# Performance work log

Measured on AMD Instinct MI355X. Metric: run time of the kernel, lower is better.

Reference implementation:

```python
import jax, jax.numpy as jnp
import numpy as np

N_NODES = 100000
N_EDGES = 1600000
N_GRAPHS = 256
IN_F = 64   # global_features (GNN input dim)
OUT_F = 64  # node_features (GNN output dim)


def setup_inputs() -> dict:
    key = jax.random.key(0)
    ks = jax.random.split(key, 8)
    x = jax.random.normal(ks[0], (N_NODES, IN_F), dtype=jnp.float32)
    edge_index = jax.random.randint(ks[1], (2, N_EDGES), 0, N_NODES, dtype=jnp.int64)
    batch = jnp.sort(jax.random.randint(ks[2], (N_NODES,), 0, N_GRAPHS, dtype=jnp.int64))
    # GNNLayer linear: in=global_features, out=node_features
    W_gnn = jax.random.normal(ks[3], (IN_F, OUT_F), dtype=jnp.float32) / np.sqrt(IN_F)
    b_gnn = jnp.zeros((OUT_F,), dtype=jnp.float32)
    # global_attention: Linear(node_features, 1)
    W_att = jax.random.normal(ks[4], (OUT_F, 1), dtype=jnp.float32) / np.sqrt(OUT_F)
    b_att = jnp.zeros((1,), dtype=jnp.float32)
    return {"x": x, "edge_index": edge_index, "batch": batch,
            "W_gnn": W_gnn, "b_gnn": b_gnn, "W_att": W_att, "b_att": b_att}


def reference(x, edge_index, batch, W_gnn, b_gnn, W_att, b_att):
    src, dst = edge_index[0], edge_index[1]
    # --- GNN message passing layer: aggregate neighbor features, transform ---
    agg = jax.ops.segment_sum(x[src], dst, num_segments=N_NODES)  # [N, IN_F]
    h = jax.nn.relu((x + agg) @ W_gnn + b_gnn)                    # [N, OUT_F]
    # --- attention scores + scatter softmax over batch segments ---
    scores = (h @ W_att + b_att)[:, 0]                            # [N]
    seg_max = jax.ops.segment_max(scores, batch, num_segments=N_GRAPHS)
    e = jnp.exp(scores - seg_max[batch])
    denom = jax.ops.segment_sum(e, batch, num_segments=N_GRAPHS)
    w = e / denom[batch]                                          # [N]
    # --- weighted scatter-add pooling ---
    out = jax.ops.segment_sum(w[:, None] * h, batch, num_segments=N_GRAPHS)
    return out  # [N_GRAPHS, OUT_F]
```

## Files before the change

### kernel.cpp

```cpp
#include <hip/hip_runtime.h>

#define N_NODES  100000
#define N_EDGES  1600000
#define N_GRAPHS 256
#define F        64

#define CHUNK    8192
#define NCHUNK   196
#define GBN      128
#define NB2      782
#define EDGE_CAP 2560

#define CAST_ELEMS   (N_NODES * F / 4)
#define CAST_BLOCKS  ((CAST_ELEMS + 1023) / 1024)
#define PREP_BLOCKS  (NCHUNK + CAST_BLOCKS)

__device__ __forceinline__ unsigned short f2bf(float f) {
    unsigned int u = __float_as_uint(f);
    u += 0x7FFFu + ((u >> 16) & 1u);
    return (unsigned short)(u >> 16);
}

__global__ __launch_bounds__(1024) void prep_kernel(
        const float* __restrict__ x, unsigned short* __restrict__ xh,
        const int* __restrict__ src, const int* __restrict__ dst,
        unsigned int* __restrict__ pairs, int* __restrict__ cstartT,
        float* __restrict__ out, float* __restrict__ denom) {
    int tid = threadIdx.x;
    int b   = blockIdx.x;

    if (b >= NCHUNK) {
        int ci = b - NCHUNK;
        if (ci == 0) {
            for (int i = tid; i < N_GRAPHS * F; i += 1024) out[i] = 0.f;
            if (tid < N_GRAPHS) denom[tid] = 0.f;
        }
        int i = ci * 1024 + tid;
        if (i < CAST_ELEMS) {
            float4 v = ((const float4*)x)[i];
            ushort4 o;
            o.x = f2bf(v.x); o.y = f2bf(v.y); o.z = f2bf(v.z); o.w = f2bf(v.w);
            ((ushort4*)xh)[i] = o;
        }
        return;
    }

    __shared__ int hist[NB2];
    __shared__ int cur[NB2];
    __shared__ int scan[1024];
    __shared__ unsigned int stage[CHUNK];
    int c    = b;
    int base = c * CHUNK;
    int m    = min(CHUNK, N_EDGES - base);

    for (int k = tid; k < NB2; k += 1024) hist[k] = 0;
    __syncthreads();
    for (int e = tid; e < m; e += 1024)
        atomicAdd(&hist[dst[base + e] >> 7], 1);
    __syncthreads();
    scan[tid] = (tid < NB2) ? hist[tid] : 0;
    __syncthreads();
    #pragma unroll
    for (int o = 1; o < 1024; o <<= 1) {
        int u = (tid >= o) ? scan[tid - o] : 0;
        __syncthreads();
        scan[tid] += u;
        __syncthreads();
    }
    if (tid < NB2) {
        int excl = scan[tid] - hist[tid];
        cur[tid] = excl;
        cstartT[tid * NCHUNK + c] = base + excl;
    }
    if (tid == 0) cstartT[NB2 * NCHUNK + c] = base + m;
    __syncthreads();
    for (int e = tid; e < m; e += 1024) {
        int d = dst[base + e];
        int slot = atomicAdd(&cur[d >> 7], 1);
        stage[slot] = ((unsigned)(d & (GBN - 1)) << 17) | (unsigned)src[base + e];
    }
    __syncthreads();
    for (int e = tid; e < m; e += 1024)
        pairs[base + e] = stage[e];
}

__global__ __launch_bounds__(512) void compact_kernel(
        const unsigned int* __restrict__ pairs,
        const int* __restrict__ cstartT,
        int* __restrict__ eidx,
        int* __restrict__ nbeg,
        int* __restrict__ nend) {
    __shared__ int rstart[NCHUNK];
    __shared__ int roff[NCHUNK + 1];
    __shared__ int sc[256];
    __shared__ unsigned int epairs[EDGE_CAP];
    __shared__ int ncnt[GBN];
    __shared__ int ncur[GBN];

    int tid   = threadIdx.x;
    int b     = blockIdx.x;
    int node0 = b * GBN;
    int nn    = min(GBN, N_NODES - node0);
    int gbase = b * EDGE_CAP;

    int myrc = 0;
    if (tid < NCHUNK) {
        int a = cstartT[b * NCHUNK + tid];
        int n = cstartT[(b + 1) * NCHUNK + tid];
        rstart[tid] = a;
        myrc = n - a;
    }
    __syncthreads();
    if (tid < 256) sc[tid] = (tid < NCHUNK) ? myrc : 0;
    __syncthreads();
    #pragma unroll
    for (int o = 1; o < 256; o <<= 1) {
        int u = (tid < 256 && tid >= o) ? sc[tid - o] : 0;
        __syncthreads();
        if (tid < 256) sc[tid] += u;
        __syncthreads();
    }
    if (tid < NCHUNK) roff[tid] = sc[tid] - myrc;
    if (tid == 0) roff[NCHUNK] = sc[NCHUNK - 1];
    __syncthreads();
    int E = roff[NCHUNK];

    for (int e = tid; e < E; e += 512) {
        int lo = 0, hi = NCHUNK - 1;
        while (lo < hi) {
            int mid = (lo + hi + 1) >> 1;
            if (roff[mid] <= e) lo = mid; else hi = mid - 1;
        }
        epairs[e] = pairs[rstart[lo] + (e - roff[lo])];
    }
    __syncthreads();

    if (tid < GBN) ncnt[tid] = 0;
    __syncthreads();
    for (int e = tid; e < E; e += 512)
        atomicAdd(&ncnt[epairs[e] >> 17], 1);
    __syncthreads();
    if (tid < 128) sc[tid] = ncnt[tid];
    __syncthreads();
    #pragma unroll
    for (int o = 1; o < 128; o <<= 1) {
        int u = (tid < 128 && tid >= o) ? sc[tid - o] : 0;
        __syncthreads();
        if (tid < 128) sc[tid] += u;
        __syncthreads();
    }
    if (tid < GBN) {
        int excl = sc[tid] - ncnt[tid];
        ncur[tid] = excl;
        if (tid < nn) {
            nbeg[node0 + tid] = gbase + excl;
            nend[node0 + tid] = gbase + excl + ncnt[tid];
        }
    }
    __syncthreads();
    for (int e = tid; e < E; e += 512) {
        unsigned int p = epairs[e];
        int slot = atomicAdd(&ncur[p >> 17], 1);
        eidx[gbase + slot] = (int)(p & 0x1FFFFu);
    }
}

#define NODES_PER_WAVE 13
#define GT_NWAVES  ((N_NODES + NODES_PER_WAVE - 1) / NODES_PER_WAVE)
#define GT_BLOCKS  ((GT_NWAVES + 3) / 4)

__device__ __forceinline__ float bfl(unsigned int u) { return __uint_as_float(u << 16); }
__device__ __forceinline__ float bfh(unsigned int u) { return __uint_as_float(u & 0xFFFF0000u); }

__global__ __launch_bounds__(256) void gather_pool_kernel(
        const unsigned short* __restrict__ xh,
        const int*   __restrict__ nbeg,
        const int*   __restrict__ nend,
        const int*   __restrict__ eidx,
        const int*   __restrict__ batch,
        const float* __restrict__ Wg,
        const float* __restrict__ bg,
        const float* __restrict__ Wa,
        const float* __restrict__ ba,
        float*       __restrict__ out_acc,
        float*       __restrict__ denom) {
    int tid  = threadIdx.x;
    int lane = tid & 63;
    int grp  = lane >> 3;
    int c    = lane & 7;
    int waveId = blockIdx.x * 4 + (tid >> 6);

    int n0 = waveId * NODES_PER_WAVE;
    if (n0 >= N_NODES) return;
    int nEnd = n0 + NODES_PER_WAVE;
    if (nEnd > N_NODES) nEnd = N_NODES;

    float wcol[F];
    #pragma unroll
    for (int k = 0; k < F; ++k) wcol[k] = Wg[k * F + lane];
    float bgl = bg[lane];
    float wal = Wa[lane];
    float ba0 = ba[0];

    const uint4* xh4 = (const uint4*)xh;

    int   cur_g = batch[n0];
    float accw  = 0.f;
    float denw  = 0.f;

    int pb = nbeg[n0];
    int pe = nend[n0];
    int sl_cur = (pb + lane < pe) ? eidx[pb + lane] : 0;

    for (int n = n0; n < nEnd; ++n) {
        int start = pb, end = pe;
        int sl    = sl_cur;
        if (n + 1 < nEnd) {
            pb = nbeg[n + 1];
            pe = nend[n + 1];
            sl_cur = (pb + lane < pe) ? eidx[pb + lane] : 0;
        }

        float a0=0.f,a1=0.f,a2=0.f,a3=0.f,a4=0.f,a5=0.f,a6=0.f,a7=0.f;
        {
            int jmax = end - start; if (jmax > 64) jmax = 64;
            for (int j = 0; j < jmax; j += 8) {
                int el = j + grp;
                int s  = __shfl(sl, el, 64);
                if (el < jmax) {
                    uint4 v = xh4[s * 8 + c];
                    a0 += bfl(v.x); a1 += bfh(v.x);
                    a2 += bfl(v.y); a3 += bfh(v.y);
                    a4 += bfl(v.z); a5 += bfh(v.z);
                    a6 += bfl(v.w); a7 += bfh(v.w);
                }
            }
        }
        for (int base = start + 64; base < end; base += 64) {
            int jmax = end - base; if (jmax > 64) jmax = 64;
            int sl2 = (base + lane < end) ? eidx[base + lane] : 0;
            for (int j = 0; j < jmax; j += 8) {
                int el = j + grp;
                int s  = __shfl(sl2, el, 64);
                if (el < jmax) {
                    uint4 v = xh4[s * 8 + c];
                    a0 += bfl(v.x); a1 += bfh(v.x);
                    a2 += bfl(v.y); a3 += bfh(v.y);
                    a4 += bfl(v.z); a5 += bfh(v.z);
                    a6 += bfl(v.w); a7 += bfh(v.w);
                }
            }
        }
        #pragma unroll
        for (int o = 8; o <= 32; o <<= 1) {
            a0 += __shfl_xor(a0, o, 64); a1 += __shfl_xor(a1, o, 64);
            a2 += __shfl_xor(a2, o, 64); a3 += __shfl_xor(a3, o, 64);
            a4 += __shfl_xor(a4, o, 64); a5 += __shfl_xor(a5, o, 64);
            a6 += __shfl_xor(a6, o, 64); a7 += __shfl_xor(a7, o, 64);
        }
        {
            uint4 v = xh4[n * 8 + c];
            a0 += bfl(v.x); a1 += bfh(v.x);
            a2 += bfl(v.y); a3 += bfh(v.y);
            a4 += bfl(v.z); a5 += bfh(v.z);
            a6 += bfl(v.w); a7 += bfh(v.w);
        }

        float re[8] = {a0,a1,a2,a3,a4,a5,a6,a7};
        float q0=0.f,q1=0.f,q2=0.f,q3=0.f,q4=0.f,q5=0.f,q6=0.f,q7=0.f;
        #pragma unroll
        for (int k = 0; k < F; k += 8) {
            int ln = k >> 3;
            q0 += __int_as_float(__builtin_amdgcn_readlane(__float_as_int(re[0]), ln)) * wcol[k + 0];
            q1 += __int_as_float(__builtin_amdgcn_readlane(__float_as_int(re[1]), ln)) * wcol[k + 1];
            q2 += __int_as_float(__builtin_amdgcn_readlane(__float_as_int(re[2]), ln)) * wcol[k + 2];
            q3 += __int_as_float(__builtin_amdgcn_readlane(__float_as_int(re[3]), ln)) * wcol[k + 3];
            q4 += __int_as_float(__builtin_amdgcn_readlane(__float_as_int(re[4]), ln)) * wcol[k + 4];
            q5 += __int_as_float(__builtin_amdgcn_readlane(__float_as_int(re[5]), ln)) * wcol[k + 5];
            q6 += __int_as_float(__builtin_amdgcn_readlane(__float_as_int(re[6]), ln)) * wcol[k + 6];
            q7 += __int_as_float(__builtin_amdgcn_readlane(__float_as_int(re[7]), ln)) * wcol[k + 7];
        }
        float hv = ((q0 + q1) + (q2 + q3)) + ((q4 + q5) + (q6 + q7)) + bgl;
        hv = hv > 0.f ? hv : 0.f;

        float p = hv * wal;
        #pragma unroll
        for (int o = 32; o > 0; o >>= 1)
            p += __shfl_down(p, o, 64);
        float s = __int_as_float(__builtin_amdgcn_readlane(__float_as_int(p), 0)) + ba0;
        float e = __expf(s);

        int g = batch[n];
        if (g != cur_g) {
            atomicAdd(&out_acc[cur_g * F + lane], accw);
            if (lane == 0) atomicAdd(&denom[cur_g], denw);
            accw = 0.f; denw = 0.f; cur_g = g;
        }
        accw += e * hv;
        denw += e;
    }
    atomicAdd(&out_acc[cur_g * F + lane], accw);
    if (lane == 0) atomicAdd(&denom[cur_g], denw);
}

__global__ __launch_bounds__(256) void finalize_kernel(
        float* __restrict__ out, const float* __restrict__ denom) {
    int i = blockIdx.x * 256 + threadIdx.x;
    if (i >= N_GRAPHS * F) return;
    float d = denom[i >> 6];
    out[i] = (d > 0.f) ? out[i] / d : 0.f;
}

extern "C" void kernel_launch(void* const* d_in, const int* in_sizes, int n_in,
                              void* d_out, int out_size, void* d_ws, size_t ws_size,
                              hipStream_t stream) {
    const float* x     = (const float*)d_in[0];
    const int*   ei    = (const int*)d_in[1];
    const int*   batch = (const int*)d_in[2];
    const float* Wg    = (const float*)d_in[3];
    const float* bg    = (const float*)d_in[4];
    const float* Wa    = (const float*)d_in[5];
    const float* ba    = (const float*)d_in[6];
    float* out = (float*)d_out;

    const int* src = ei;
    const int* dst = ei + N_EDGES;

    char* ws = (char*)d_ws;
    unsigned short* xh      = (unsigned short*)(ws);
    unsigned int*   pairs   = (unsigned int*)(ws + 12800000);
    int*            cstartT = (int*)(ws + 19200000);
    int*            eidx    = (int*)(ws + 19814144);
    int*            nbeg    = (int*)(ws + 27821824);
    int*            nend    = (int*)(ws + 28221824);
    float*          denom   = (float*)(ws + 28621824);

    prep_kernel       <<<PREP_BLOCKS, 1024, 0, stream>>>(
        x, xh, src, dst, pairs, cstartT, out, denom);
    compact_kernel    <<<NB2, 512, 0, stream>>>(pairs, cstartT, eidx, nbeg, nend);
    gather_pool_kernel<<<GT_BLOCKS, 256, 0, stream>>>(
        xh, nbeg, nend, eidx, batch, Wg, bg, Wa, ba, out, denom);
    finalize_kernel   <<<(N_GRAPHS * F + 255) / 256, 256, 0, stream>>>(out, denom);
}
```

Baseline: 197.1 us.

## Fuse all four kernels into one cooperative persistent kernel with grid syncs

Merges the prep, compact, gather-pool and finalize kernels into a single cooperative kernel. Each phase runs as a grid-stride loop over a persistent grid, with grid-wide barriers between phases, and the phases share one LDS union. The aim is to remove kernel launch gaps and tail effects. In exchange, the gather phase now runs at 1024 threads per block, with 64 weight registers per thread and occupancy-limited residency, which may lower latency hiding. If maxB*256 exceeds the device's resident capacity, the cooperative launch may fail.

```diff
diff --git a/kernel.cpp b/kernel.cpp
--- a/kernel.cpp
+++ b/kernel.cpp
@@ -1,4 +1,7 @@
 #include <hip/hip_runtime.h>
+#include <hip/hip_cooperative_groups.h>
+
+namespace cg = cooperative_groups;
 
 #define N_NODES  100000
 #define N_EDGES  1600000
@@ -11,304 +14,295 @@
 #define NB2      782
 #define EDGE_CAP 2560
 
-#define CAST_ELEMS   (N_NODES * F / 4)
-#define CAST_BLOCKS  ((CAST_ELEMS + 1023) / 1024)
-#define PREP_BLOCKS  (NCHUNK + CAST_BLOCKS)
+#define CAST_ELEMS (N_NODES * F / 4)
+#define NCHK16     ((N_NODES + 15) / 16)
 
 __device__ __forceinline__ unsigned short f2bf(float f) {
     unsigned int u = __float_as_uint(f);
     u += 0x7FFFu + ((u >> 16) & 1u);
     return (unsigned short)(u >> 16);
 }
-
-__global__ __launch_bounds__(1024) void prep_kernel(
-        const float* __restrict__ x, unsigned short* __restrict__ xh,
+__device__ __forceinline__ float bfl(unsigned int u) { return __uint_as_float(u << 16); }
+__device__ __forceinline__ float bfh(unsigned int u) { return __uint_as_float(u & 0xFFFF0000u); }
+
+union PhaseLDS {
+    struct {
+        int hist[NB2];
+        int cur[NB2];
+        int scan[1024];
+        unsigned int stage[CHUNK];
+    } p;
+    struct {
+        int rstart[NCHUNK];
+        int roff[NCHUNK + 1];
+        int sc[256];
+        unsigned int epairs[EDGE_CAP];
+        int ncnt[GBN];
+        int ncur[GBN];
+    } c;
+};
+
+__global__ __launch_bounds__(1024) void mega_kernel(
+        const float* __restrict__ x,
+        unsigned short* __restrict__ xh,
         const int* __restrict__ src, const int* __restrict__ dst,
         unsigned int* __restrict__ pairs, int* __restrict__ cstartT,
+        int* __restrict__ eidx, int* __restrict__ nbeg, int* __restrict__ nend,
+        const int* __restrict__ batch,
+        const float* __restrict__ Wg, const float* __restrict__ bg,
+        const float* __restrict__ Wa, const float* __restrict__ ba,
         float* __restrict__ out, float* __restrict__ denom) {
+    cg::grid_group grid = cg::this_grid();
+    __shared__ PhaseLDS sh;
     int tid = threadIdx.x;
-    int b   = blockIdx.x;
-
-    if (b >= NCHUNK) {
-        int ci = b - NCHUNK;
+    int nB  = gridDim.x;
+
+    for (int c = blockIdx.x; c < NCHUNK; c += nB) {
+        int base = c * CHUNK;
+        int m    = min(CHUNK, N_EDGES - base);
+        for (int k = tid; k < NB2; k += 1024) sh.p.hist[k] = 0;
+        __syncthreads();
+        for (int e = tid; e < m; e += 1024)
+            atomicAdd(&sh.p.hist[dst[base + e] >> 7], 1);
+        __syncthreads();
+        sh.p.scan[tid] = (tid < NB2) ? sh.p.hist[tid] : 0;
+        __syncthreads();
+        #pragma unroll
+        for (int o = 1; o < 1024; o <<= 1) {
+            int u = (tid >= o) ? sh.p.scan[tid - o] : 0;
+            __syncthreads();
+            sh.p.scan[tid] += u;
+            __syncthreads();
+        }
+        if (tid < NB2) {
+            int excl = sh.p.scan[tid] - sh.p.hist[tid];
+            sh.p.cur[tid] = excl;
+            cstartT[tid * NCHUNK + c] = base + excl;
+        }
+        if (tid == 0) cstartT[NB2 * NCHUNK + c] = base + m;
+        __syncthreads();
+        for (int e = tid; e < m; e += 1024) {
+            int d = dst[base + e];
+            int slot = atomicAdd(&sh.p.cur[d >> 7], 1);
+            sh.p.stage[slot] = ((unsigned)(d & (GBN - 1)) << 17) | (unsigned)src[base + e];
+        }
+        __syncthreads();
+        for (int e = tid; e < m; e += 1024)
+            pairs[base + e] = sh.p.stage[e];
+        __syncthreads();
+    }
+    if (blockIdx.x >= NCHUNK) {
+        int castBlocks = nB - NCHUNK;
+        int ci = blockIdx.x - NCHUNK;
         if (ci == 0) {
             for (int i = tid; i < N_GRAPHS * F; i += 1024) out[i] = 0.f;
             if (tid < N_GRAPHS) denom[tid] = 0.f;
         }
-        int i = ci * 1024 + tid;
-        if (i < CAST_ELEMS) {
+        for (int i = ci * 1024 + tid; i < CAST_ELEMS; i += castBlocks * 1024) {
             float4 v = ((const float4*)x)[i];
             ushort4 o;
             o.x = f2bf(v.x); o.y = f2bf(v.y); o.z = f2bf(v.z); o.w = f2bf(v.w);
             ((ushort4*)xh)[i] = o;
         }
-        return;
-    }
-
-    __shared__ int hist[NB2];
-    __shared__ int cur[NB2];
-    __shared__ int scan[1024];
-    __shared__ unsigned int stage[CHUNK];
-    int c    = b;
-    int base = c * CHUNK;
-    int m    = min(CHUNK, N_EDGES - base);
-
-    for (int k = tid; k < NB2; k += 1024) hist[k] = 0;
-    __syncthreads();
-    for (int e = tid; e < m; e += 1024)
-        atomicAdd(&hist[dst[base + e] >> 7], 1);
-    __syncthreads();
-    scan[tid] = (tid < NB2) ? hist[tid] : 0;
-    __syncthreads();
-    #pragma unroll
-    for (int o = 1; o < 1024; o <<= 1) {
-        int u = (tid >= o) ? scan[tid - o] : 0;
-        __syncthreads();
-        scan[tid] += u;
-        __syncthreads();
-    }
-    if (tid < NB2) {
-        int excl = scan[tid] - hist[tid];
-        cur[tid] = excl;
-        cstartT[tid * NCHUNK + c] = base + excl;
-    }
-    if (tid == 0) cstartT[NB2 * NCHUNK + c] = base + m;
-    __syncthreads();
-    for (int e = tid; e < m; e += 1024) {
-        int d = dst[base + e];
-        int slot = atomicAdd(&cur[d >> 7], 1);
-        stage[slot] = ((unsigned)(d & (GBN - 1)) << 17) | (unsigned)src[base + e];
-    }
-    __syncthreads();
-    for (int e = tid; e < m; e += 1024)
-        pairs[base + e] = stage[e];
-}
-
-__global__ __launch_bounds__(512) void compact_kernel(
-        const unsigned int* __restrict__ pairs,
-        const int* __restrict__ cstartT,
-        int* __restrict__ eidx,
-        int* __restrict__ nbeg,
-        int* __restrict__ nend) {
-    __shared__ int rstart[NCHUNK];
-    __shared__ int roff[NCHUNK + 1];
-    __shared__ int sc[256];
-    __shared__ unsigned int epairs[EDGE_CAP];
-    __shared__ int ncnt[GBN];
-    __shared__ int ncur[GBN];
-
-    int tid   = threadIdx.x;
-    int b     = blockIdx.x;
-    int node0 = b * GBN;
-    int nn    = min(GBN, N_NODES - node0);
-    int gbase = b * EDGE_CAP;
-
-    int myrc = 0;
-    if (tid < NCHUNK) {
-        int a = cstartT[b * NCHUNK + tid];
-        int n = cstartT[(b + 1) * NCHUNK + tid];
-        rstart[tid] = a;
-        myrc = n - a;
-    }
-    __syncthreads();
-    if (tid < 256) sc[tid] = (tid < NCHUNK) ? myrc : 0;
-    __syncthreads();
-    #pragma unroll
-    for (int o = 1; o < 256; o <<= 1) {
-        int u = (tid < 256 && tid >= o) ? sc[tid - o] : 0;
-        __syncthreads();
-        if (tid < 256) sc[tid] += u;
-        __syncthreads();
-    }
-    if (tid < NCHUNK) roff[tid] = sc[tid] - myrc;
-    if (tid == 0) roff[NCHUNK] = sc[NCHUNK - 1];
-    __syncthreads();
-    int E = roff[NCHUNK];
-
-    for (int e = tid; e < E; e += 512) {
-        int lo = 0, hi = NCHUNK - 1;
-        while (lo < hi) {
-            int mid = (lo + hi + 1) >> 1;
-            if (roff[mid] <= e) lo = mid; else hi = mid - 1;
-        }
-        epairs[e] = pairs[rstart[lo] + (e - roff[lo])];
-    }
-    __syncthreads();
-
-    if (tid < GBN) ncnt[tid] = 0;
-    __syncthreads();
-    for (int e = tid; e < E; e += 512)
-        atomicAdd(&ncnt[epairs[e] >> 17], 1);
-    __syncthreads();
-    if (tid < 128) sc[tid] = ncnt[tid];
-    __syncthreads();
-    #pragma unroll
-    for (int o = 1; o < 128; o <<= 1) {
-        int u = (tid < 128 && tid >= o) ? sc[tid - o] : 0;
-        __syncthreads();
-        if (tid < 128) sc[tid] += u;
-        __syncthreads();
-    }
-    if (tid < GBN) {
-        int excl = sc[tid] - ncnt[tid];
-        ncur[tid] = excl;
-        if (tid < nn) {
-            nbeg[node0 + tid] = gbase + excl;
-            nend[node0 + tid] = gbase + excl + ncnt[tid];
-        }
-    }
-    __syncthreads();
-    for (int e = tid; e < E; e += 512) {
-        unsigned int p = epairs[e];
-        int slot = atomicAdd(&ncur[p >> 17], 1);
-        eidx[gbase + slot] = (int)(p & 0x1FFFFu);
-    }
-}
-
-#define NODES_PER_WAVE 13
-#define GT_NWAVES  ((N_NODES + NODES_PER_WAVE - 1) / NODES_PER_WAVE)
-#define GT_BLOCKS  ((GT_NWAVES + 3) / 4)
-
-__device__ __forceinline__ float bfl(unsigned int u) { return __uint_as_float(u << 16); }
-__device__ __forceinline__ float bfh(unsigned int u) { return __uint_as_float(u & 0xFFFF0000u); }
-
-__global__ __launch_bounds__(256) void gather_pool_kernel(
-        const unsigned short* __restrict__ xh,
-        const int*   __restrict__ nbeg,
-        const int*   __restrict__ nend,
-        const int*   __restrict__ eidx,
-        const int*   __restrict__ batch,
-        const float* __restrict__ Wg,
-        const float* __restrict__ bg,
-        const float* __restrict__ Wa,
-        const float* __restrict__ ba,
-        float*       __restrict__ out_acc,
-        float*       __restrict__ denom) {
-    int tid  = threadIdx.x;
-    int lane = tid & 63;
-    int grp  = lane >> 3;
-    int c    = lane & 7;
-    int waveId = blockIdx.x * 4 + (tid >> 6);
-
-    int n0 = waveId * NODES_PER_WAVE;
-    if (n0 >= N_NODES) return;
-    int nEnd = n0 + NODES_PER_WAVE;
-    if (nEnd > N_NODES) nEnd = N_NODES;
-
-    float wcol[F];
-    #pragma unroll
-    for (int k = 0; k < F; ++k) wcol[k] = Wg[k * F + lane];
-    float bgl = bg[lane];
-    float wal = Wa[lane];
-    float ba0 = ba[0];
-
-    const uint4* xh4 = (const uint4*)xh;
-
-    int   cur_g = batch[n0];
-    float accw  = 0.f;
-    float denw  = 0.f;
-
-    int pb = nbeg[n0];
-    int pe = nend[n0];
-    int sl_cur = (pb + lane < pe) ? eidx[pb + lane] : 0;
-
-    for (int n = n0; n < nEnd; ++n) {
-        int start = pb, end = pe;
-        int sl    = sl_cur;
-        if (n + 1 < nEnd) {
-            pb = nbeg[n + 1];
-            pe = nend[n + 1];
-            sl_cur = (pb + lane < pe) ? eidx[pb + lane] : 0;
-        }
-
-        float a0=0.f,a1=0.f,a2=0.f,a3=0.f,a4=0.f,a5=0.f,a6=0.f,a7=0.f;
-        {
-            int jmax = end - start; if (jmax > 64) jmax = 64;
-            for (int j = 0; j < jmax; j += 8) {
-                int el = j + grp;
-                int s  = __shfl(sl, el, 64);
-                if (el < jmax) {
-                    uint4 v = xh4[s * 8 + c];
+    }
+    __threadfence();
+    grid.sync();
+
+    for (int b = blockIdx.x; b < NB2; b += nB) {
+        int node0 = b * GBN;
+        int nn    = min(GBN, N_NODES - node0);
+        int gbase = b * EDGE_CAP;
+
+        int myrc = 0;
+        if (tid < NCHUNK) {
+            int a = cstartT[b * NCHUNK + tid];
+            int n = cstartT[(b + 1) * NCHUNK + tid];
+            sh.c.rstart[tid] = a;
+            myrc = n - a;
+        }
+        __syncthreads();
+        if (tid < 256) sh.c.sc[tid] = (tid < NCHUNK) ? myrc : 0;
+        __syncthreads();
+        #pragma unroll
+        for (int o = 1; o < 256; o <<= 1) {
+            int u = (tid < 256 && tid >= o) ? sh.c.sc[tid - o] : 0;
+            __syncthreads();
+            if (tid < 256) sh.c.sc[tid] += u;
+            __syncthreads();
+        }
+        if (tid < NCHUNK) sh.c.roff[tid] = sh.c.sc[tid] - myrc;
+        if (tid == 0) sh.c.roff[NCHUNK] = sh.c.sc[NCHUNK - 1];
+        __syncthreads();
+        int E = sh.c.roff[NCHUNK];
+
+        for (int e = tid; e < E; e += 1024) {
+            int lo = 0, hi = NCHUNK - 1;
+            while (lo < hi) {
+                int mid = (lo + hi + 1) >> 1;
+                if (sh.c.roff[mid] <= e) lo = mid; else hi = mid - 1;
+            }
+            sh.c.epairs[e] = pairs[sh.c.rstart[lo] + (e - sh.c.roff[lo])];
+        }
+        __syncthreads();
+        if (tid < GBN) sh.c.ncnt[tid] = 0;
+        __syncthreads();
+        for (int e = tid; e < E; e += 1024)
+            atomicAdd(&sh.c.ncnt[sh.c.epairs[e] >> 17], 1);
+        __syncthreads();
+        if (tid < 128) sh.c.sc[tid] = sh.c.ncnt[tid];
+        __syncthreads();
+        #pragma unroll
+        for (int o = 1; o < 128; o <<= 1) {
+            int u = (tid < 128 && tid >= o) ? sh.c.sc[tid - o] : 0;
+            __syncthreads();
+            if (tid < 128) sh.c.sc[tid] += u;
+            __syncthreads();
+        }
+        if (tid < GBN) {
+            int excl = sh.c.sc[tid] - sh.c.ncnt[tid];
+            sh.c.ncur[tid] = excl;
+            if (tid < nn) {
+                nbeg[node0 + tid] = gbase + excl;
+                nend[node0 + tid] = gbase + excl + sh.c.ncnt[tid];
+            }
+        }
+        __syncthreads();
+        for (int e = tid; e < E; e += 1024) {
+            unsigned int p = sh.c.epairs[e];
+            int slot = atomicAdd(&sh.c.ncur[p >> 17], 1);
+            eidx[gbase + slot] = (int)(p & 0x1FFFFu);
+        }
+        __syncthreads();
+    }
+    __threadfence();
+    grid.sync();
+
+    {
+        int lane = tid & 63;
+        int grp  = lane >> 3;
+        int c    = lane & 7;
+        int waveId     = blockIdx.x * 16 + (tid >> 6);
+        int totalWaves = nB * 16;
+
+        float bgl = bg[lane];
+        float wal = Wa[lane];
+        float ba0 = ba[0];
+        float wcol[F];
+        #pragma unroll
+        for (int k = 0; k < F; ++k) wcol[k] = Wg[k * F + lane];
+
+        const uint4* xh4 = (const uint4*)xh;
+
+        for (int t = waveId; t < NCHK16; t += totalWaves) {
+            int n0   = t * 16;
+            int nEnd = min(n0 + 16, N_NODES);
+
+            int   cur_g = batch[n0];
+            float accw  = 0.f;
+            float denw  = 0.f;
+
+            int pb = nbeg[n0];
+            int pe = nend[n0];
+            int sl_cur = (pb + lane < pe) ? eidx[pb + lane] : 0;
+
+            for (int n = n0; n < nEnd; ++n) {
+                int start = pb, end = pe;
+                int sl    = sl_cur;
+                if (n + 1 < nEnd) {
+                    pb = nbeg[n + 1];
+                    pe = nend[n + 1];
+                    sl_cur = (pb + lane < pe) ? eidx[pb + lane] : 0;
+                }
+
+                float a0=0.f,a1=0.f,a2=0.f,a3=0.f,a4=0.f,a5=0.f,a6=0.f,a7=0.f;
+                {
+                    int jmax = end - start; if (jmax > 64) jmax = 64;
+                    for (int j = 0; j < jmax; j += 8) {
+                        int el = j + grp;
+                        int s  = __shfl(sl, el, 64);
+                        if (el < jmax) {
+                            uint4 v = xh4[s * 8 + c];
+                            a0 += bfl(v.x); a1 += bfh(v.x);
+                            a2 += bfl(v.y); a3 += bfh(v.y);
+                            a4 += bfl(v.z); a5 += bfh(v.z);
+                            a6 += bfl(v.w); a7 += bfh(v.w);
+                        }
+                    }
+                }
+                for (int base = start + 64; base < end; base += 64) {
+                    int jmax = end - base; if (jmax > 64) jmax = 64;
+                    int sl2 = (base + lane < end) ? eidx[base + lane] : 0;
+                    for (int j = 0; j < jmax; j += 8) {
+                        int el = j + grp;
+                        int s  = __shfl(sl2, el, 64);
+                        if (el < jmax) {
+                            uint4 v = xh4[s * 8 + c];
+                            a0 += bfl(v.x); a1 += bfh(v.x);
+                            a2 += bfl(v.y); a3 += bfh(v.y);
+                            a4 += bfl(v.z); a5 += bfh(v.z);
+                            a6 += bfl(v.w); a7 += bfh(v.w);
+                        }
+                    }
+                }
+                #pragma unroll
+                for (int o = 8; o <= 32; o <<= 1) {
+                    a0 += __shfl_xor(a0, o, 64); a1 += __shfl_xor(a1, o, 64);
+                    a2 += __shfl_xor(a2, o, 64); a3 += __shfl_xor(a3, o, 64);
+                    a4 += __shfl_xor(a4, o, 64); a5 += __shfl_xor(a5, o, 64);
+                    a6 += __shfl_xor(a6, o, 64); a7 += __shfl_xor(a7, o, 64);
+                }
+                {
+                    uint4 v = xh4[n * 8 + c];
                     a0 += bfl(v.x); a1 += bfh(v.x);
                     a2 += bfl(v.y); a3 += bfh(v.y);
                     a4 += bfl(v.z); a5 += bfh(v.z);
                     a6 += bfl(v.w); a7 += bfh(v.w);
                 }
+
+                float re[8] = {a0,a1,a2,a3,a4,a5,a6,a7};
+                float q0=0.f,q1=0.f,q2=0.f,q3=0.f,q4=0.f,q5=0.f,q6=0.f,q7=0.f;
+                #pragma unroll
+                for (int k = 0; k < F; k += 8) {
+                    int ln = k >> 3;
+                    q0 += __int_as_float(__builtin_amdgcn_readlane(__float_as_int(re[0]), ln)) * wcol[k + 0];
+                    q1 += __int_as_float(__builtin_amdgcn_readlane(__float_as_int(re[1]), ln)) * wcol[k + 1];
+                    q2 += __int_as_float(__builtin_amdgcn_readlane(__float_as_int(re[2]), ln)) * wcol[k + 2];
+                    q3 += __int_as_float(__builtin_amdgcn_readlane(__float_as_int(re[3]), ln)) * wcol[k + 3];
+                    q4 += __int_as_float(__builtin_amdgcn_readlane(__float_as_int(re[4]), ln)) * wcol[k + 4];
+                    q5 += __int_as_float(__builtin_amdgcn_readlane(__float_as_int(re[5]), ln)) * wcol[k + 5];
+                    q6 += __int_as_float(__builtin_amdgcn_readlane(__float_as_int(re[6]), ln)) * wcol[k + 6];
+                    q7 += __int_as_float(__builtin_amdgcn_readlane(__float_as_int(re[7]), ln)) * wcol[k + 7];
+                }
+                float hv = ((q0 + q1) + (q2 + q3)) + ((q4 + q5) + (q6 + q7)) + bgl;
+                hv = hv > 0.f ? hv : 0.f;
+
+                float p = hv * wal;
+                #pragma unroll
+                for (int o = 32; o > 0; o >>= 1)
+                    p += __shfl_down(p, o, 64);
+                float s = __int_as_float(__builtin_amdgcn_readlane(__float_as_int(p), 0)) + ba0;
+                float e = __expf(s);
+
+                int g = batch[n];
+                if (g != cur_g) {
+                    atomicAdd(&out[cur_g * F + lane], accw);
+                    if (lane == 0) atomicAdd(&denom[cur_g], denw);
+                    accw = 0.f; denw = 0.f; cur_g = g;
+                }
+                accw += e * hv;
+                denw += e;
             }
-        }
-        for (int base = start + 64; base < end; base += 64) {
-            int jmax = end - base; if (jmax > 64) jmax = 64;
-            int sl2 = (base + lane < end) ? eidx[base + lane] : 0;
-            for (int j = 0; j < jmax; j += 8) {
-                int el = j + grp;
-                int s  = __shfl(sl2, el, 64);
-                if (el < jmax) {
-                    uint4 v = xh4[s * 8 + c];
-                    a0 += bfl(v.x); a1 += bfh(v.x);
-                    a2 += bfl(v.y); a3 += bfh(v.y);
-                    a4 += bfl(v.z); a5 += bfh(v.z);
-                    a6 += bfl(v.w); a7 += bfh(v.w);
-                }
-            }
-        }
-        #pragma unroll
-        for (int o = 8; o <= 32; o <<= 1) {
-            a0 += __shfl_xor(a0, o, 64); a1 += __shfl_xor(a1, o, 64);
-            a2 += __shfl_xor(a2, o, 64); a3 += __shfl_xor(a3, o, 64);
-            a4 += __shfl_xor(a4, o, 64); a5 += __shfl_xor(a5, o, 64);
-            a6 += __shfl_xor(a6, o, 64); a7 += __shfl_xor(a7, o, 64);
-        }
-        {
-            uint4 v = xh4[n * 8 + c];
-            a0 += bfl(v.x); a1 += bfh(v.x);
-            a2 += bfl(v.y); a3 += bfh(v.y);
-            a4 += bfl(v.z); a5 += bfh(v.z);
-            a6 += bfl(v.w); a7 += bfh(v.w);
-        }
-
-        float re[8] = {a0,a1,a2,a3,a4,a5,a6,a7};
-        float q0=0.f,q1=0.f,q2=0.f,q3=0.f,q4=0.f,q5=0.f,q6=0.f,q7=0.f;
-        #pragma unroll
-        for (int k = 0; k < F; k += 8) {
-            int ln = k >> 3;
-            q0 += __int_as_float(__builtin_amdgcn_readlane(__float_as_int(re[0]), ln)) * wcol[k + 0];
-            q1 += __int_as_float(__builtin_amdgcn_readlane(__float_as_int(re[1]), ln)) * wcol[k + 1];
-            q2 += __int_as_float(__builtin_amdgcn_readlane(__float_as_int(re[2]), ln)) * wcol[k + 2];
-            q3 += __int_as_float(__builtin_amdgcn_readlane(__float_as_int(re[3]), ln)) * wcol[k + 3];
-            q4 += __int_as_float(__builtin_amdgcn_readlane(__float_as_int(re[4]), ln)) * wcol[k + 4];
-            q5 += __int_as_float(__builtin_amdgcn_readlane(__float_as_int(re[5]), ln)) * wcol[k + 5];
-            q6 += __int_as_float(__builtin_amdgcn_readlane(__float_as_int(re[6]), ln)) * wcol[k + 6];
-            q7 += __int_as_float(__builtin_amdgcn_readlane(__float_as_int(re[7]), ln)) * wcol[k + 7];
-        }
-        float hv = ((q0 + q1) + (q2 + q3)) + ((q4 + q5) + (q6 + q7)) + bgl;
-        hv = hv > 0.f ? hv : 0.f;
-
-        float p = hv * wal;
-        #pragma unroll
-        for (int o = 32; o > 0; o >>= 1)
-            p += __shfl_down(p, o, 64);
-        float s = __int_as_float(__builtin_amdgcn_readlane(__float_as_int(p), 0)) + ba0;
-        float e = __expf(s);
-
-        int g = batch[n];
-        if (g != cur_g) {
-            atomicAdd(&out_acc[cur_g * F + lane], accw);
+            atomicAdd(&out[cur_g * F + lane], accw);
             if (lane == 0) atomicAdd(&denom[cur_g], denw);
-            accw = 0.f; denw = 0.f; cur_g = g;
-        }
-        accw += e * hv;
-        denw += e;
-    }
-    atomicAdd(&out_acc[cur_g * F + lane], accw);
-    if (lane == 0) atomicAdd(&denom[cur_g], denw);
-}
-
-__global__ __launch_bounds__(256) void finalize_kernel(
-        float* __restrict__ out, const float* __restrict__ denom) {
-    int i = blockIdx.x * 256 + threadIdx.x;
-    if (i >= N_GRAPHS * F) return;
-    float d = denom[i >> 6];
-    out[i] = (d > 0.f) ? out[i] / d : 0.f;
+        }
+    }
+    __threadfence();
+    grid.sync();
+
+    for (int i = blockIdx.x * 1024 + tid; i < N_GRAPHS * F; i += nB * 1024) {
+        float d = denom[i >> 6];
+        out[i] = (d > 0.f) ? out[i] / d : 0.f;
+    }
 }
 
 extern "C" void kernel_launch(void* const* d_in, const int* in_sizes, int n_in,
@@ -335,10 +329,18 @@
     int*            nend    = (int*)(ws + 28221824);
     float*          denom   = (float*)(ws + 28621824);
 
-    prep_kernel       <<<PREP_BLOCKS, 1024, 0, stream>>>(
-        x, xh, src, dst, pairs, cstartT, out, denom);
-    compact_kernel    <<<NB2, 512, 0, stream>>>(pairs, cstartT, eidx, nbeg, nend);
-    gather_pool_kernel<<<GT_BLOCKS, 256, 0, stream>>>(
-        xh, nbeg, nend, eidx, batch, Wg, bg, Wa, ba, out, denom);
-    finalize_kernel   <<<(N_GRAPHS * F + 255) / 256, 256, 0, stream>>>(out, denom);
+    int maxB = 0;
+    hipOccupancyMaxActiveBlocksPerMultiprocessor(&maxB, mega_kernel, 1024, 0);
+    if (maxB < 1) maxB = 1;
+    int grid = maxB * 256;
+    if (grid > 512) grid = 512;
+
+    void* args[] = {
+        (void*)&x, (void*)&xh, (void*)&src, (void*)&dst,
+        (void*)&pairs, (void*)&cstartT, (void*)&eidx, (void*)&nbeg, (void*)&nend,
+        (void*)&batch, (void*)&Wg, (void*)&bg, (void*)&Wa, (void*)&ba,
+        (void*)&out, (void*)&denom
+    };
+    hipLaunchCooperativeKernel((void*)mega_kernel, dim3(grid), dim3(1024),
+                               args, 0, stream);
 }
```

Result: slower. 561.4 us (+184.8%).
